# Kernel tuning notes

Measured on AMD Instinct MI355X. Metric: run time of the kernel, lower is better.

The kernel has to match this reference:

```python
import jax, jax.numpy as jnp
import numpy as np

N, E, H, L, T, NH = 20000, 200000, 128, 10, 2, 4


def _ln(x, g, b, eps=1e-5):
    mu = jnp.mean(x, -1, keepdims=True)
    d = x - mu
    v = jnp.mean(d * d, -1, keepdims=True)
    return d * jax.lax.rsqrt(v + eps) * g + b


def _mha(q_in, kv_in, wqkv, bqkv, wo, bo, nh=NH):
    # torch nn.MultiheadAttention (batch=1, eval mode)
    Hd = q_in.shape[-1]
    d = Hd // nh
    wq, wk, wv = jnp.split(wqkv, 3, axis=1)
    bq, bk, bv = jnp.split(bqkv, 3)
    q = (q_in @ wq + bq).reshape(-1, nh, d)
    k = (kv_in @ wk + bk).reshape(-1, nh, d)
    v = (kv_in @ wv + bv).reshape(-1, nh, d)
    s = jnp.einsum('qhd,khd->hqk', q, k) / jnp.sqrt(jnp.float32(d))
    a = jax.nn.softmax(s, axis=-1)
    o = jnp.einsum('hqk,khd->qhd', a, v).reshape(-1, Hd)
    return o @ wo + bo


def setup_inputs() -> dict:
    key = jax.random.key(0)
    ks = iter(jax.random.split(key, 64))
    def rn(shape, scale=1.0):
        return jax.random.normal(next(ks), shape, jnp.float32) * scale
    s = 0.05
    inp = {}
    inp['x'] = rn((N, H))
    inp['edge_index'] = jax.random.randint(next(ks), (2, E), 0, N)
    inp['edge_attr'] = rn((E, H))
    # per-layer edge MLP: Linear(3H,2H) LN GELU Linear(2H,H) LN
    inp['edge_w1'] = rn((L, 3 * H, 2 * H), s); inp['edge_b1'] = jnp.zeros((L, 2 * H))
    inp['edge_ln1g'] = jnp.ones((L, 2 * H)); inp['edge_ln1b'] = jnp.zeros((L, 2 * H))
    inp['edge_w2'] = rn((L, 2 * H, H), s); inp['edge_b2'] = jnp.zeros((L, H))
    inp['edge_ln2g'] = jnp.ones((L, H)); inp['edge_ln2b'] = jnp.zeros((L, H))
    # per-layer node MLP: Linear(3H,2H) LN GELU Linear(2H,H) LN
    inp['node_w1'] = rn((L, 3 * H, 2 * H), s); inp['node_b1'] = jnp.zeros((L, 2 * H))
    inp['node_ln1g'] = jnp.ones((L, 2 * H)); inp['node_ln1b'] = jnp.zeros((L, 2 * H))
    inp['node_w2'] = rn((L, 2 * H, H), s); inp['node_b2'] = jnp.zeros((L, H))
    inp['node_ln2g'] = jnp.ones((L, H)); inp['node_ln2b'] = jnp.zeros((L, H))
    # GlobalTokenTransformer (shared across layers)
    inp['token_embed'] = rn((T, H), 0.02)
    inp['tok_wqkv'] = rn((H, 3 * H), s); inp['tok_bqkv'] = jnp.zeros(3 * H)
    inp['tok_wo'] = rn((H, H), s); inp['tok_bo'] = jnp.zeros(H)
    inp['ln_t1g'] = jnp.ones(H); inp['ln_t1b'] = jnp.zeros(H)
    inp['ln_t2g'] = jnp.ones(H); inp['ln_t2b'] = jnp.zeros(H)
    inp['ff_w1'] = rn((H, 4 * H), s); inp['ff_b1'] = jnp.zeros(4 * H)
    inp['ff_w2'] = rn((4 * H, H), s); inp['ff_b2'] = jnp.zeros(H)
    inp['nod_wqkv'] = rn((H, 3 * H), s); inp['nod_bqkv'] = jnp.zeros(3 * H)
    inp['nod_wo'] = rn((H, H), s); inp['nod_bo'] = jnp.zeros(H)
    return inp


def reference(x, edge_index, edge_attr,
              edge_w1, edge_b1, edge_ln1g, edge_ln1b, edge_w2, edge_b2, edge_ln2g, edge_ln2b,
              node_w1, node_b1, node_ln1g, node_ln1b, node_w2, node_b2, node_ln2g, node_ln2b,
              token_embed, tok_wqkv, tok_bqkv, tok_wo, tok_bo,
              ln_t1g, ln_t1b, ln_t2g, ln_t2b, ff_w1, ff_b1, ff_w2, ff_b2,
              nod_wqkv, nod_bqkv, nod_wo, nod_bo):
    row, col = edge_index[0], edge_index[1]
    n = x.shape[0]
    e = edge_index.shape[1]
    # in-degree counts for scatter-mean (identical every layer)
    deg = jnp.clip(jax.ops.segment_sum(jnp.ones((e,), x.dtype), col, num_segments=n), 1.0)[:, None]

    def global_ctx(nodes):
        tokens = token_embed  # [T, H]
        t = _mha(tokens, nodes, tok_wqkv, tok_bqkv, tok_wo, tok_bo)
        tokens = _ln(tokens + t, ln_t1g, ln_t1b)
        ff = jax.nn.gelu(tokens @ ff_w1 + ff_b1, approximate=False) @ ff_w2 + ff_b2
        tokens = _ln(tokens + ff, ln_t2g, ln_t2b)
        return _mha(nodes, tokens, nod_wqkv, nod_bqkv, nod_wo, nod_bo)  # [N, H]

    for i in range(L):
        # edge update: gather -> MLP -> residual
        ei = jnp.concatenate([x[row], x[col], edge_attr], axis=1)  # [E, 3H]
        h = jax.nn.gelu(_ln(ei @ edge_w1[i] + edge_b1[i], edge_ln1g[i], edge_ln1b[i]), approximate=False)
        edge_attr = edge_attr + _ln(h @ edge_w2[i] + edge_b2[i], edge_ln2g[i], edge_ln2b[i])
        # scatter-mean aggregation at destination nodes
        agg = jax.ops.segment_sum(edge_attr, col, num_segments=n) / deg
        ctx = global_ctx(x)
        ni = jnp.concatenate([x, agg, ctx], axis=1)  # [N, 3H]
        h = jax.nn.gelu(_ln(ni @ node_w1[i] + node_b1[i], node_ln1g[i], node_ln1b[i]), approximate=False)
        x = x + _ln(h @ node_w2[i] + node_b2[i], node_ln2g[i], node_ln2b[i])
    return (x, edge_attr)
```

## Files before the change

kernel.cpp:

```cpp
#include <hip/hip_runtime.h>
#include <math.h>

#define Nn 20000
#define Ee 200000
#define Hh 128
#define Ll 10

using short8  = __attribute__((ext_vector_type(8))) short;
using floatx4 = __attribute__((ext_vector_type(4))) float;

__device__ __forceinline__ float bf2f(unsigned short u){ return __uint_as_float(((unsigned)u)<<16); }
__device__ __forceinline__ unsigned short f2bf(float f){
  unsigned u = __float_as_uint(f);
  u += 0x7FFF + ((u>>16)&1);
  return (unsigned short)(u>>16);
}
__device__ __forceinline__ float gelu_f(float x){
  float x3 = x*x*x;
  float z = 1.595769122f*x + 0.071354816f*x3;
  return x / (1.0f + __expf(-z));
}

template<bool GATHER>
__global__ __launch_bounds__(256, 2)
void mlp_fused(const unsigned short* __restrict__ s0,
               const unsigned short* __restrict__ s1,
               const unsigned short* __restrict__ s2b,
               const float* __restrict__ s2f,
               const int* __restrict__ rowI, const int* __restrict__ colI,
               const unsigned short* __restrict__ w1p,
               const unsigned short* __restrict__ w2p,
               const float* __restrict__ pb1, const float* __restrict__ pg1,
               const float* __restrict__ pbb1,
               const float* __restrict__ pb2, const float* __restrict__ pg2,
               const float* __restrict__ pbb2,
               float* __restrict__ resf,
               unsigned short* __restrict__ resb,
               float* __restrict__ agg,
               int M)
{
  __shared__ __align__(16) unsigned short wbuf[2][8192];
  __shared__ __align__(16) unsigned short lds_h[4][16*264];
  __shared__ float lds_par[1152];

  const int tid = threadIdx.x;
  const int w = tid>>6, lane = tid&63, l16 = lane&15, q = lane>>4;
  const int R0 = blockIdx.x*64;

  for (int u = tid; u < 1152; u += 256){
    float v;
    if      (u <  256) v = pb1[u];
    else if (u <  512) v = pg1[u-256];
    else if (u <  768) v = pbb1[u-512];
    else if (u <  896) v = pb2[u-768];
    else if (u < 1024) v = pg2[u-896];
    else               v = pbb2[u-1024];
    lds_par[u] = v;
  }

  {
    const unsigned short* src = w1p;
    #pragma unroll
    for (int i=0;i<4;++i)
      *(short8*)&wbuf[0][tid*8 + i*2048] = *(const short8*)(src + tid*8 + i*2048);
  }

  const int gA = R0 + w*16 + l16;

  short8 af[12];
  if (GATHER){
    const unsigned short* p0 = s0 + (size_t)rowI[gA]*Hh + q*8;
    const unsigned short* p1 = s1 + (size_t)colI[gA]*Hh + q*8;
    const float*          p2 = s2f + (size_t)gA*Hh + q*8;
    #pragma unroll
    for (int c=0;c<4;++c){
      af[c]   = *(const short8*)(p0 + c*32);
      af[4+c] = *(const short8*)(p1 + c*32);
      float4 u0 = *(const float4*)(p2 + c*32);
      float4 u1 = *(const float4*)(p2 + c*32 + 4);
      short8 t8;
      t8[0]=(short)f2bf(u0.x); t8[1]=(short)f2bf(u0.y);
      t8[2]=(short)f2bf(u0.z); t8[3]=(short)f2bf(u0.w);
      t8[4]=(short)f2bf(u1.x); t8[5]=(short)f2bf(u1.y);
      t8[6]=(short)f2bf(u1.z); t8[7]=(short)f2bf(u1.w);
      af[8+c] = t8;
    }
  } else {
    int gg = gA < M ? gA : (M-1);
    const unsigned short* p0 = s0 + (size_t)gg*Hh + q*8;
    const unsigned short* p1 = s1 + (size_t)gg*Hh + q*8;
    const unsigned short* p2 = s2b + (size_t)gg*Hh + q*8;
    #pragma unroll
    for (int c=0;c<4;++c){
      af[c]   = *(const short8*)(p0 + c*32);
      af[4+c] = *(const short8*)(p1 + c*32);
      af[8+c] = *(const short8*)(p2 + c*32);
    }
  }

  __syncthreads();

  const floatx4 fz = {0.f,0.f,0.f,0.f};
  floatx4 acc1[16];
  #pragma unroll
  for (int t=0;t<16;++t) acc1[t] = fz;

  #pragma unroll
  for (int c=0;c<12;++c){
    const int sel = c&1, nsel = (c+1)&1;
    short8 nx0, nx1, nx2, nx3;
    if (c < 11){
      const unsigned short* src = w1p + (size_t)(c+1)*8192;
      nx0 = *(const short8*)(src + tid*8);
      nx1 = *(const short8*)(src + tid*8 + 2048);
      nx2 = *(const short8*)(src + tid*8 + 4096);
      nx3 = *(const short8*)(src + tid*8 + 6144);
    } else {
      const unsigned short* src = w2p;
      nx0 = *(const short8*)(src + tid*8);
      nx1 = *(const short8*)(src + tid*8 + 2048);
    }
    #pragma unroll
    for (int t=0;t<16;++t){
      short8 bf = *(const short8*)&wbuf[sel][t*512 + lane*8];
      acc1[t] = __builtin_amdgcn_mfma_f32_16x16x32_bf16(af[c], bf, acc1[t], 0,0,0);
    }
    if (c < 11){
      *(short8*)&wbuf[nsel][tid*8]        = nx0;
      *(short8*)&wbuf[nsel][tid*8 + 2048] = nx1;
      *(short8*)&wbuf[nsel][tid*8 + 4096] = nx2;
      *(short8*)&wbuf[nsel][tid*8 + 6144] = nx3;
    } else {
      *(short8*)&wbuf[0][tid*8]        = nx0;
      *(short8*)&wbuf[0][tid*8 + 2048] = nx1;
    }
    __syncthreads();
  }

  #pragma unroll
  for (int r=0;r<4;++r){
    float hv[16];
    float s=0.f, ss=0.f;
    #pragma unroll
    for (int t=0;t<16;++t){
      float v = acc1[t][r] + lds_par[t*16+l16];
      hv[t]=v; s+=v; ss+=v*v;
    }
    #pragma unroll
    for (int m=1;m<16;m<<=1){ s += __shfl_xor(s,m); ss += __shfl_xor(ss,m); }
    float mean = s*(1.f/256.f);
    float var  = ss*(1.f/256.f) - mean*mean;
    float rstd = rsqrtf(var + 1e-5f);
    int ro = q*4 + r;
    #pragma unroll
    for (int t=0;t<16;++t){
      int col = t*16+l16;
      float hh = (hv[t]-mean)*rstd*lds_par[256+col] + lds_par[512+col];
      lds_h[w][ro*264 + col] = f2bf(gelu_f(hh));
    }
  }

  floatx4 acc2[8];
  #pragma unroll
  for (int t=0;t<8;++t) acc2[t] = fz;

  #pragma unroll
  for (int c=0;c<8;++c){
    const int sel = c&1, nsel = (c+1)&1;
    short8 nx0, nx1;
    if (c < 7){
      const unsigned short* src = w2p + (size_t)(c+1)*4096;
      nx0 = *(const short8*)(src + tid*8);
      nx1 = *(const short8*)(src + tid*8 + 2048);
    }
    short8 a2 = *(const short8*)&lds_h[w][l16*264 + c*32 + q*8];
    #pragma unroll
    for (int t=0;t<8;++t){
      short8 bf = *(const short8*)&wbuf[sel][t*512 + lane*8];
      acc2[t] = __builtin_amdgcn_mfma_f32_16x16x32_bf16(a2, bf, acc2[t], 0,0,0);
    }
    if (c < 7){
      *(short8*)&wbuf[nsel][tid*8]        = nx0;
      *(short8*)&wbuf[nsel][tid*8 + 2048] = nx1;
    }
    __syncthreads();
  }

  #pragma unroll
  for (int r=0;r<4;++r){
    float vv[8];
    float s=0.f, ss=0.f;
    #pragma unroll
    for (int t=0;t<8;++t){
      float v = acc2[t][r] + lds_par[768 + t*16+l16];
      vv[t]=v; s+=v; ss+=v*v;
    }
    #pragma unroll
    for (int m=1;m<16;m<<=1){ s += __shfl_xor(s,m); ss += __shfl_xor(ss,m); }
    float mean = s*(1.f/128.f);
    float var  = ss*(1.f/128.f) - mean*mean;
    float rstd = rsqrtf(var + 1e-5f);
    int g = R0 + w*16 + q*4 + r;
    if (g < M){
      int cn = 0;
      if (GATHER) cn = colI[g];
      #pragma unroll
      for (int t=0;t<8;++t){
        int col = t*16+l16;
        float outv = (vv[t]-mean)*rstd*lds_par[896+col] + lds_par[1024+col];
        size_t idx = (size_t)g*Hh + col;
        float nv = resf[idx] + outv;
        resf[idx] = nv;
        if (!GATHER) resb[idx] = f2bf(nv);
        if (GATHER)  atomicAdd(&agg[(size_t)cn*Hh + col], nv);
      }
    }
  }
}

template<int NCOLS>
__global__ __launch_bounds__(256, 4)
void gemm_bias(const unsigned short* __restrict__ A,
               const unsigned short* __restrict__ Wp,
               const float* __restrict__ bias,
               unsigned short* __restrict__ out,
               int M)
{
  constexpr int NT = NCOLS/16;
  const int tid = threadIdx.x;
  const int w = tid>>6, lane = tid&63, l16 = lane&15, q = lane>>4;
  const int R0 = blockIdx.x*64;
  int gA = R0 + w*16 + l16;
  int ga = gA < M ? gA : (M-1);
  const unsigned short* ap = A + (size_t)ga*128 + q*8;

  const floatx4 fz = {0.f,0.f,0.f,0.f};
  floatx4 acc[NT];
  #pragma unroll
  for (int t=0;t<NT;++t) acc[t] = fz;

  const unsigned short* wl = Wp + (size_t)lane*8;
  #pragma unroll
  for (int c=0;c<4;++c){
    short8 af = *(const short8*)(ap + c*32);
    #pragma unroll
    for (int t=0;t<NT;++t){
      short8 bf = *(const short8*)(wl + (size_t)(c*NT+t)*512);
      acc[t] = __builtin_amdgcn_mfma_f32_16x16x32_bf16(af, bf, acc[t], 0,0,0);
    }
  }
  #pragma unroll
  for (int r=0;r<4;++r){
    int g = R0 + w*16 + q*4 + r;
    if (g < M){
      #pragma unroll
      for (int t=0;t<NT;++t){
        int col = t*16+l16;
        out[(size_t)g*NCOLS + col] = f2bf(acc[t][r] + bias[col]);
      }
    }
  }
}

__global__ __launch_bounds__(256, 2)
void attn_reduce(const unsigned short* __restrict__ kv, const float* __restrict__ tq,
                 float* __restrict__ onum, float* __restrict__ denom, int Nv)
{
  __shared__ float sbuf[8][256];
  __shared__ float qs[256];
  int tid = threadIdx.x;
  qs[tid] = tq[tid];
  __syncthreads();
  int base = blockIdx.x*256;
  int i = base + tid;
  float ex[8];
  if (i < Nv){
    const unsigned short* kr = kv + (size_t)i*256;
    float acc[8];
    #pragma unroll
    for (int a=0;a<8;++a) acc[a]=0.f;
    #pragma unroll
    for (int d8=0; d8<16; ++d8){
      short8 k8 = *(const short8*)(kr + d8*8);
      #pragma unroll
      for (int u=0;u<8;++u){
        int d = d8*8+u;
        float kd = bf2f((unsigned short)k8[u]);
        int h = d>>5;
        acc[h]   += qs[d]*kd;
        acc[4+h] += qs[128+d]*kd;
      }
    }
    #pragma unroll
    for (int a=0;a<8;++a) ex[a] = expf(acc[a]*0.17677669529663688f);
  } else {
    #pragma unroll
    for (int a=0;a<8;++a) ex[a]=0.f;
  }
  #pragma unroll
  for (int a=0;a<8;++a) sbuf[a][tid] = ex[a];
  __syncthreads();
  int th = tid>>5, d = tid&31, h = th&3;
  int cnt = Nv - base; if (cnt > 256) cnt = 256;
  float accv = 0.f, dsum = 0.f;
  #pragma unroll 4
  for (int j=0;j<cnt;++j){
    float wgt = sbuf[th][j];
    accv += wgt * bf2f(kv[(size_t)(base+j)*256 + 128 + h*32 + d]);
    dsum += wgt;
  }
  atomicAdd(&onum[th*32+d], accv);
  if (d==0) atomicAdd(&denom[th], dsum);
}

__global__ void token_kernel(const float* __restrict__ onum, const float* __restrict__ denom,
  const float* __restrict__ tok_wo, const float* __restrict__ tok_bo,
  const float* __restrict__ token_embed,
  const float* __restrict__ g1, const float* __restrict__ b1,
  const float* __restrict__ g2, const float* __restrict__ b2,
  const float* __restrict__ ff_w1, const float* __restrict__ ff_b1,
  const float* __restrict__ ff_w2, const float* __restrict__ ff_b2,
  const float* __restrict__ nod_wqkv, const float* __restrict__ nod_bqkv,
  float* __restrict__ kv2)
{
  __shared__ float O[2][128];
  __shared__ float T[2][128];
  __shared__ float F[2][512];
  __shared__ float stats[4];
  int tid = threadIdx.x;
  int t = tid>>7, c = tid&127;
  {
    int th = t*4 + (c>>5);
    O[t][c] = onum[th*32 + (c&31)] / denom[th];
  }
  __syncthreads();
  {
    float s = tok_bo[c];
    for (int k=0;k<128;++k) s += O[t][k]*tok_wo[k*128+c];
    T[t][c] = token_embed[t*128+c] + s;
  }
  __syncthreads();
  if (tid < 2){
    float s=0.f, ss=0.f;
    for (int k=0;k<128;++k){ float v=T[tid][k]; s+=v; ss+=v*v; }
    float m = s*(1.f/128.f);
    stats[tid*2] = m;
    stats[tid*2+1] = rsqrtf(ss*(1.f/128.f)-m*m+1e-5f);
  }
  __syncthreads();
  T[t][c] = (T[t][c]-stats[t*2])*stats[t*2+1]*g1[c] + b1[c];
  __syncthreads();
  for (int u=0;u<4;++u){
    int o = tid + u*256;
    int tt = o>>9, j = o&511;
    float s = ff_b1[j];
    for (int k=0;k<128;++k) s += T[tt][k]*ff_w1[k*512+j];
    F[tt][j] = gelu_f(s);
  }
  __syncthreads();
  {
    float s = ff_b2[c];
    for (int k=0;k<512;++k) s += F[t][k]*ff_w2[k*128+c];
    O[t][c] = T[t][c] + s;
  }
  __syncthreads();
  if (tid < 2){
    float s=0.f, ss=0.f;
    for (int k=0;k<128;++k){ float v=O[tid][k]; s+=v; ss+=v*v; }
    float m = s*(1.f/128.f);
    stats[tid*2] = m;
    stats[tid*2+1] = rsqrtf(ss*(1.f/128.f)-m*m+1e-5f);
  }
  __syncthreads();
  O[t][c] = (O[t][c]-stats[t*2])*stats[t*2+1]*g2[c] + b2[c];
  __syncthreads();
  for (int u=0;u<2;++u){
    int o = tid + u*256;
    int tt = o>>8, cc = o&255;
    float s = nod_bqkv[128+cc];
    for (int k=0;k<128;++k) s += O[tt][k]*nod_wqkv[k*384+128+cc];
    if (cc < 128) kv2[tt*128+cc] = s;
    else          kv2[256 + tt*128 + (cc-128)] = s;
  }
}

__global__ void node_attn(const unsigned short* __restrict__ qn,
                          const float* __restrict__ kv2,
                          unsigned short* __restrict__ attn, int Nv)
{
  __shared__ float k2s[256], v2s[256];
  int tid = threadIdx.x;
  k2s[tid] = kv2[tid];
  v2s[tid] = kv2[256+tid];
  __syncthreads();
  int g = blockIdx.x*8 + (tid>>5);
  int d = tid&31;
  int i = g>>2, h = g&3;
  if (i >= Nv) return;
  int c = h*32+d;
  float qv = bf2f(qn[(size_t)i*128 + c]);
  float p0 = qv * k2s[c];
  float p1 = qv * k2s[128+c];
  #pragma unroll
  for (int m=1;m<32;m<<=1){ p0 += __shfl_xor(p0,m); p1 += __shfl_xor(p1,m); }
  float e0 = expf(p0*0.17677669529663688f);
  float e1 = expf(p1*0.17677669529663688f);
  float outv = (e0*v2s[c] + e1*v2s[128+c]) / (e0+e1);
  attn[(size_t)i*128 + c] = f2bf(outv);
}

__global__ void prep_weights(const float* __restrict__ ew1,
  const float* __restrict__ ew2,
  const float* __restrict__ nw1,
  const float* __restrict__ nw2,
  const float* __restrict__ tok_wqkv,
  const float* __restrict__ nod_wqkv,
  const float* __restrict__ nod_wo,
  const float* __restrict__ token_embed,
  const float* __restrict__ tok_bqkv,
  unsigned short* __restrict__ ew1p, unsigned short* __restrict__ ew2p,
  unsigned short* __restrict__ nw1p, unsigned short* __restrict__ nw2p,
  unsigned short* __restrict__ kvp, unsigned short* __restrict__ qnp,
  unsigned short* __restrict__ wop, float* __restrict__ tq)
{
  int gid = blockIdx.x*256 + threadIdx.x;
  if (gid < Ll*98304){
    int l = gid / 98304; int idx = gid % 98304;
    int c = idx >> 13;
    int t = (idx >> 9) & 15;
    int lane = (idx >> 3) & 63;
    int j = idx & 7;
    int k = c*32 + (lane>>4)*8 + j;
    int n = t*16 + (lane&15);
    size_t src = (size_t)l*98304 + (size_t)k*256 + n;
    ew1p[gid] = f2bf(ew1[src]);
    nw1p[gid] = f2bf(nw1[src]);
  }
  if (gid < Ll*32768){
    int l = gid / 32768; int idx = gid % 32768;
    int c = idx >> 12;
    int t = (idx >> 9) & 7;
    int lane = (idx >> 3) & 63;
    int j = idx & 7;
    int k = c*32 + (lane>>4)*8 + j;
    int n = t*16 + (lane&15);
    size_t src = (size_t)l*32768 + (size_t)k*128 + n;
    ew2p[gid] = f2bf(ew2[src]);
    nw2p[gid] = f2bf(nw2[src]);
  }
  if (gid < 32768){
    int c = gid >> 13;
    int t = (gid >> 9) & 15;
    int lane = (gid >> 3) & 63;
    int j = gid & 7;
    int k = c*32 + (lane>>4)*8 + j;
    int n = t*16 + (lane&15);
    kvp[gid] = f2bf(tok_wqkv[(size_t)k*384 + 128 + n]);
  }
  if (gid < 16384){
    int c = gid >> 12;
    int t = (gid >> 9) & 7;
    int lane = (gid >> 3) & 63;
    int j = gid & 7;
    int k = c*32 + (lane>>4)*8 + j;
    int n = t*16 + (lane&15);
    qnp[gid] = f2bf(nod_wqkv[(size_t)k*384 + n]);
    wop[gid] = f2bf(nod_wo[(size_t)k*128 + n]);
  }
  if (gid < 256){
    int t = gid >> 7, c = gid & 127;
    float s = tok_bqkv[c];
    for (int k=0;k<128;++k) s += token_embed[t*128+k] * tok_wqkv[k*384+c];
    tq[gid] = s;
  }
}

__global__ void init_state(const float* __restrict__ x_in,
  const float* __restrict__ e_in,
  float* __restrict__ x_f32, float* __restrict__ e_f32,
  unsigned short* __restrict__ x_b16)
{
  size_t gid = (size_t)blockIdx.x*256 + threadIdx.x;
  if (gid < (size_t)Ee*Hh) e_f32[gid] = e_in[gid];
  if (gid < (size_t)Nn*Hh){
    float v = x_in[gid];
    x_f32[gid] = v;
    x_b16[gid] = f2bf(v);
  }
}

__global__ void deg_count(const int* __restrict__ colI, int* __restrict__ cnt){
  int gid = blockIdx.x*256+threadIdx.x;
  if (gid < Ee) atomicAdd(&cnt[colI[gid]], 1);
}
__global__ void deg_inv(const int* __restrict__ cnt, float* __restrict__ inv){
  int gid = blockIdx.x*256+threadIdx.x;
  if (gid < Nn){ int c = cnt[gid]; inv[gid] = 1.0f / (float)(c > 1 ? c : 1); }
}
__global__ void agg_fin(const float* __restrict__ agg, const float* __restrict__ inv,
                        unsigned short* __restrict__ aggb){
  size_t gid = (size_t)blockIdx.x*256+threadIdx.x;
  if (gid < (size_t)Nn*Hh) aggb[gid] = f2bf(agg[gid] * inv[gid>>7]);
}

extern "C" void kernel_launch(void* const* d_in, const int* in_sizes, int n_in,
                              void* d_out, int out_size, void* d_ws, size_t ws_size,
                              hipStream_t stream)
{
  const float* x_in       = (const float*)d_in[0];
  const int*   eidx       = (const int*)d_in[1];
  const float* e_in       = (const float*)d_in[2];
  const float* edge_w1    = (const float*)d_in[3];
  const float* edge_b1    = (const float*)d_in[4];
  const float* edge_ln1g  = (const float*)d_in[5];
  const float* edge_ln1b  = (const float*)d_in[6];
  const float* edge_w2    = (const float*)d_in[7];
  const float* edge_b2    = (const float*)d_in[8];
  const float* edge_ln2g  = (const float*)d_in[9];
  const float* edge_ln2b  = (const float*)d_in[10];
  const float* node_w1    = (const float*)d_in[11];
  const float* node_b1    = (const float*)d_in[12];
  const float* node_ln1g  = (const float*)d_in[13];
  const float* node_ln1b  = (const float*)d_in[14];
  const float* node_w2    = (const float*)d_in[15];
  const float* node_b2    = (const float*)d_in[16];
  const float* node_ln2g  = (const float*)d_in[17];
  const float* node_ln2b  = (const float*)d_in[18];
  const float* token_embed= (const float*)d_in[19];
  const float* tok_wqkv   = (const float*)d_in[20];
  const float* tok_bqkv   = (const float*)d_in[21];
  const float* tok_wo     = (const float*)d_in[22];
  const float* tok_bo     = (const float*)d_in[23];
  const float* ln_t1g     = (const float*)d_in[24];
  const float* ln_t1b     = (const float*)d_in[25];
  const float* ln_t2g     = (const float*)d_in[26];
  const float* ln_t2b     = (const float*)d_in[27];
  const float* ff_w1      = (const float*)d_in[28];
  const float* ff_b1      = (const float*)d_in[29];
  const float* ff_w2      = (const float*)d_in[30];
  const float* ff_b2      = (const float*)d_in[31];
  const float* nod_wqkv   = (const float*)d_in[32];
  const float* nod_bqkv   = (const float*)d_in[33];
  const float* nod_wo     = (const float*)d_in[34];
  const float* nod_bo     = (const float*)d_in[35];

  const int* rowI = eidx;
  const int* colI = eidx + Ee;

  float* out_x = (float*)d_out;
  float* out_e = out_x + (size_t)Nn*Hh;

  char* base = (char*)d_ws;
  size_t off = 0;
  auto alloc = [&](size_t bytes)->char*{
    char* p = base + off; off += (bytes + 255) & ~(size_t)255; return p;
  };
  unsigned short* x_b16 = (unsigned short*)alloc((size_t)Nn*Hh*2);
  float*          agg_f = (float*)alloc((size_t)Nn*Hh*4);
  unsigned short* agg_b = (unsigned short*)alloc((size_t)Nn*Hh*2);
  unsigned short* ctx_b = (unsigned short*)alloc((size_t)Nn*Hh*2);
  unsigned short* kv_b  = (unsigned short*)alloc((size_t)Nn*256*2);
  unsigned short* qn_b  = (unsigned short*)alloc((size_t)Nn*Hh*2);
  unsigned short* at_b  = (unsigned short*)alloc((size_t)Nn*Hh*2);
  float*          invd  = (float*)alloc((size_t)Nn*4);
  int*            dcnt  = (int*)alloc((size_t)Nn*4);
  unsigned short* ew1p  = (unsigned short*)alloc((size_t)Ll*98304*2);
  unsigned short* ew2p  = (unsigned short*)alloc((size_t)Ll*32768*2);
  unsigned short* nw1p  = (unsigned short*)alloc((size_t)Ll*98304*2);
  unsigned short* nw2p  = (unsigned short*)alloc((size_t)Ll*32768*2);
  unsigned short* kvp   = (unsigned short*)alloc((size_t)32768*2);
  unsigned short* qnp   = (unsigned short*)alloc((size_t)16384*2);
  unsigned short* wop   = (unsigned short*)alloc((size_t)16384*2);
  float*          tq    = (float*)alloc(256*4);
  float*          kv2   = (float*)alloc(512*4);
  float*          onum  = (float*)alloc(264*4);
  float*          denom = onum + 256;
  if (off > ws_size) return;

  hipMemsetAsync(dcnt, 0, (size_t)Nn*4, stream);
  prep_weights<<<(Ll*98304 + 255)/256, 256, 0, stream>>>(
      edge_w1, edge_w2, node_w1, node_w2, tok_wqkv, nod_wqkv, nod_wo,
      token_embed, tok_bqkv, ew1p, ew2p, nw1p, nw2p, kvp, qnp, wop, tq);
  init_state<<<(int)(((size_t)Ee*Hh + 255)/256), 256, 0, stream>>>(
      x_in, e_in, out_x, out_e, x_b16);
  deg_count<<<(Ee+255)/256, 256, 0, stream>>>(colI, dcnt);
  deg_inv<<<(Nn+255)/256, 256, 0, stream>>>(dcnt, invd);

  for (int l = 0; l < Ll; ++l){
    hipMemsetAsync(agg_f, 0, (size_t)Nn*Hh*4, stream);
    hipMemsetAsync(onum, 0, 264*4, stream);

    mlp_fused<true><<<Ee/64, 256, 0, stream>>>(x_b16, x_b16, nullptr, out_e,
        rowI, colI,
        ew1p + (size_t)l*98304, ew2p + (size_t)l*32768,
        edge_b1 + l*256, edge_ln1g + l*256, edge_ln1b + l*256,
        edge_b2 + l*128, edge_ln2g + l*128, edge_ln2b + l*128,
        out_e, nullptr, agg_f, Ee);
    agg_fin<<<(int)(((size_t)Nn*Hh + 255)/256), 256, 0, stream>>>(agg_f, invd, agg_b);

    gemm_bias<256><<<(Nn+63)/64, 256, 0, stream>>>(x_b16, kvp, tok_bqkv+128, kv_b, Nn);
    attn_reduce<<<(Nn+255)/256, 256, 0, stream>>>(kv_b, tq, onum, denom, Nn);
    token_kernel<<<1, 256, 0, stream>>>(onum, denom, tok_wo, tok_bo, token_embed,
        ln_t1g, ln_t1b, ln_t2g, ln_t2b, ff_w1, ff_b1, ff_w2, ff_b2,
        nod_wqkv, nod_bqkv, kv2);
    gemm_bias<128><<<(Nn+63)/64, 256, 0, stream>>>(x_b16, qnp, nod_bqkv, qn_b, Nn);
    node_attn<<<(Nn*4 + 7)/8, 256, 0, stream>>>(qn_b, kv2, at_b, Nn);
    gemm_bias<128><<<(Nn+63)/64, 256, 0, stream>>>(at_b, wop, nod_bo, ctx_b, Nn);

    mlp_fused<false><<<(Nn+63)/64, 256, 0, stream>>>(x_b16, agg_b, ctx_b, nullptr,
        nullptr, nullptr,
        nw1p + (size_t)l*98304, nw2p + (size_t)l*32768,
        node_b1 + l*256, node_ln1g + l*256, node_ln1b + l*256,
        node_b2 + l*128, node_ln2g + l*128, node_ln2b + l*128,
        out_x, x_b16, nullptr, Nn);
  }
}
```

Measured before the change: 4.100 ms.

## Replace atomic scatter-mean with CSR-based gather aggregation

The change removes the per-element float atomicAdd scatter from the edge MLP epilogue. It builds a CSR index of edges grouped by destination node once, and adds a gather kernel in which one wavefront per node sums its incoming edge rows and writes the bf16 mean. This drops the per-layer memset of the fp32 aggregation buffer and the finalize kernel, and avoids atomic contention. The cost is an extra pass that re-reads the updated edge features (about 100MB per layer) with indirect, uncoalesced row accesses.

```diff
diff --git a/kernel.cpp b/kernel.cpp
--- a/kernel.cpp
+++ b/kernel.cpp
@@ -36,7 +36,6 @@
                const float* __restrict__ pbb2,
                float* __restrict__ resf,
                unsigned short* __restrict__ resb,
-               float* __restrict__ agg,
                int M)
 {
   __shared__ __align__(16) unsigned short wbuf[2][8192];
@@ -202,8 +201,6 @@
     float rstd = rsqrtf(var + 1e-5f);
     int g = R0 + w*16 + q*4 + r;
     if (g < M){
-      int cn = 0;
-      if (GATHER) cn = colI[g];
       #pragma unroll
       for (int t=0;t<8;++t){
         int col = t*16+l16;
@@ -212,10 +209,70 @@
         float nv = resf[idx] + outv;
         resf[idx] = nv;
         if (!GATHER) resb[idx] = f2bf(nv);
-        if (GATHER)  atomicAdd(&agg[(size_t)cn*Hh + col], nv);
       }
     }
   }
+}
+
+__global__ void csr_prefix(const int* __restrict__ cnt, int* __restrict__ rowPtr)
+{
+  __shared__ int part[256];
+  const int tid = threadIdx.x;
+  const int CH = (Nn + 255)/256;
+  int c0 = tid*CH; if (c0 > Nn) c0 = Nn;
+  int c1 = c0+CH;  if (c1 > Nn) c1 = Nn;
+  int s = 0;
+  for (int i=c0;i<c1;++i) s += cnt[i];
+  part[tid] = s;
+  __syncthreads();
+  for (int d=1; d<256; d<<=1){
+    int v = (tid>=d) ? part[tid-d] : 0;
+    __syncthreads();
+    part[tid] += v;
+    __syncthreads();
+  }
+  int off = part[tid] - s;
+  for (int i=c0;i<c1;++i){ rowPtr[i] = off; off += cnt[i]; }
+  if (tid == 255) rowPtr[Nn] = off;
+}
+
+__global__ void csr_fill(const int* __restrict__ colI, const int* __restrict__ rowPtr,
+                         int* __restrict__ cursor, int* __restrict__ elist)
+{
+  int e = blockIdx.x*256 + threadIdx.x;
+  if (e < Ee){
+    int n = colI[e];
+    int p = atomicAdd(&cursor[n], 1);
+    elist[rowPtr[n] + p] = e;
+  }
+}
+
+__global__ __launch_bounds__(256, 8)
+void agg_gather(const float* __restrict__ ef, const int* __restrict__ rowPtr,
+                const int* __restrict__ elist, const float* __restrict__ invd,
+                unsigned short* __restrict__ aggb)
+{
+  int n = blockIdx.x*4 + (threadIdx.x>>6);
+  int lane = threadIdx.x & 63;
+  if (n >= Nn) return;
+  int j0 = rowPtr[n], j1 = rowPtr[n+1];
+  float s0=0.f, s1=0.f, t0=0.f, t1=0.f;
+  int j = j0;
+  for (; j+1 < j1; j += 2){
+    int e0 = elist[j], e1 = elist[j+1];
+    float2 a = *(const float2*)(ef + (size_t)e0*Hh + lane*2);
+    float2 b = *(const float2*)(ef + (size_t)e1*Hh + lane*2);
+    s0 += a.x; s1 += a.y; t0 += b.x; t1 += b.y;
+  }
+  if (j < j1){
+    int e0 = elist[j];
+    float2 a = *(const float2*)(ef + (size_t)e0*Hh + lane*2);
+    s0 += a.x; s1 += a.y;
+  }
+  s0 += t0; s1 += t1;
+  float iv = invd[n];
+  unsigned int packed = ((unsigned)f2bf(s1*iv) << 16) | (unsigned)f2bf(s0*iv);
+  *(unsigned int*)&aggb[(size_t)n*Hh + lane*2] = packed;
 }
 
 template<int NCOLS>
@@ -496,11 +553,6 @@
 __global__ void deg_inv(const int* __restrict__ cnt, float* __restrict__ inv){
   int gid = blockIdx.x*256+threadIdx.x;
   if (gid < Nn){ int c = cnt[gid]; inv[gid] = 1.0f / (float)(c > 1 ? c : 1); }
-}
-__global__ void agg_fin(const float* __restrict__ agg, const float* __restrict__ inv,
-                        unsigned short* __restrict__ aggb){
-  size_t gid = (size_t)blockIdx.x*256+threadIdx.x;
-  if (gid < (size_t)Nn*Hh) aggb[gid] = f2bf(agg[gid] * inv[gid>>7]);
 }
 
 extern "C" void kernel_launch(void* const* d_in, const int* in_sizes, int n_in,
@@ -556,7 +608,6 @@
     char* p = base + off; off += (bytes + 255) & ~(size_t)255; return p;
   };
   unsigned short* x_b16 = (unsigned short*)alloc((size_t)Nn*Hh*2);
-  float*          agg_f = (float*)alloc((size_t)Nn*Hh*4);
   unsigned short* agg_b = (unsigned short*)alloc((size_t)Nn*Hh*2);
   unsigned short* ctx_b = (unsigned short*)alloc((size_t)Nn*Hh*2);
   unsigned short* kv_b  = (unsigned short*)alloc((size_t)Nn*256*2);
@@ -564,6 +615,9 @@
   unsigned short* at_b  = (unsigned short*)alloc((size_t)Nn*Hh*2);
   float*          invd  = (float*)alloc((size_t)Nn*4);
   int*            dcnt  = (int*)alloc((size_t)Nn*4);
+  int*            rowP  = (int*)alloc((size_t)(Nn+1)*4);
+  int*            curs  = (int*)alloc((size_t)Nn*4);
+  int*            elist = (int*)alloc((size_t)Ee*4);
   unsigned short* ew1p  = (unsigned short*)alloc((size_t)Ll*98304*2);
   unsigned short* ew2p  = (unsigned short*)alloc((size_t)Ll*32768*2);
   unsigned short* nw1p  = (unsigned short*)alloc((size_t)Ll*98304*2);
@@ -578,16 +632,18 @@
   if (off > ws_size) return;
 
   hipMemsetAsync(dcnt, 0, (size_t)Nn*4, stream);
+  hipMemsetAsync(curs, 0, (size_t)Nn*4, stream);
   prep_weights<<<(Ll*98304 + 255)/256, 256, 0, stream>>>(
       edge_w1, edge_w2, node_w1, node_w2, tok_wqkv, nod_wqkv, nod_wo,
       token_embed, tok_bqkv, ew1p, ew2p, nw1p, nw2p, kvp, qnp, wop, tq);
   init_state<<<(int)(((size_t)Ee*Hh + 255)/256), 256, 0, stream>>>(
       x_in, e_in, out_x, out_e, x_b16);
   deg_count<<<(Ee+255)/256, 256, 0, stream>>>(colI, dcnt);
+  csr_prefix<<<1, 256, 0, stream>>>(dcnt, rowP);
   deg_inv<<<(Nn+255)/256, 256, 0, stream>>>(dcnt, invd);
+  csr_fill<<<(Ee+255)/256, 256, 0, stream>>>(colI, rowP, curs, elist);
 
   for (int l = 0; l < Ll; ++l){
-    hipMemsetAsync(agg_f, 0, (size_t)Nn*Hh*4, stream);
     hipMemsetAsync(onum, 0, 264*4, stream);
 
     mlp_fused<true><<<Ee/64, 256, 0, stream>>>(x_b16, x_b16, nullptr, out_e,
@@ -595,8 +651,8 @@
         ew1p + (size_t)l*98304, ew2p + (size_t)l*32768,
         edge_b1 + l*256, edge_ln1g + l*256, edge_ln1b + l*256,
         edge_b2 + l*128, edge_ln2g + l*128, edge_ln2b + l*128,
-        out_e, nullptr, agg_f, Ee);
-    agg_fin<<<(int)(((size_t)Nn*Hh + 255)/256), 256, 0, stream>>>(agg_f, invd, agg_b);
+        out_e, nullptr, Ee);
+    agg_gather<<<(Nn+3)/4, 256, 0, stream>>>(out_e, rowP, elist, invd, agg_b);
 
     gemm_bias<256><<<(Nn+63)/64, 256, 0, stream>>>(x_b16, kvp, tok_bqkv+128, kv_b, Nn);
     attn_reduce<<<(Nn+255)/256, 256, 0, stream>>>(kv_b, tq, onum, denom, Nn);
@@ -612,6 +668,6 @@
         nw1p + (size_t)l*98304, nw2p + (size_t)l*32768,
         node_b1 + l*256, node_ln1g + l*256, node_ln1b + l*256,
         node_b2 + l*128, node_ln2g + l*128, node_ln2b + l*128,
-        out_x, x_b16, nullptr, Nn);
-  }
-}
+        out_x, x_b16, Nn);
+  }
+}
```

Result: faster. 3.526 ms (-14.0%).
